# Kernel optimization log

Measured on AMD Instinct MI355X. Metric: run time of the kernel, lower is better.

Reference implementation:

```python
import jax, jax.numpy as jnp
import numpy as np

B, D, H, O = 8192, 1024, 1024, 1024
LN_EPS = 1e-6  # flax LayerNorm default


def setup_inputs() -> dict:
    key = jax.random.key(0)
    ks = jax.random.split(key, 18)
    s_i = 1.0 / np.sqrt(D)  # lecun_normal-ish scale, fan_in = D
    s_h = 1.0 / np.sqrt(H)
    inp = {
        "x": jax.random.normal(ks[0], (B, D), jnp.float32),
        "h": jax.random.normal(ks[1], (B, H), jnp.float32),
        # input projections (use_bias=True)
        "Wir": jax.random.normal(ks[2], (D, H), jnp.float32) * s_i,
        "bir": jax.random.normal(ks[3], (H,), jnp.float32) * 0.01,
        "Wiz": jax.random.normal(ks[4], (D, H), jnp.float32) * s_i,
        "biz": jnp.zeros((H,), jnp.float32),  # chrono_init with T_min=None -> zeros
        "Win": jax.random.normal(ks[5], (D, H), jnp.float32) * s_i,
        "bin_": jax.random.normal(ks[6], (H,), jnp.float32) * 0.01,
        # hidden projections (hr, hz: no bias; hn: bias)
        "Whr": jax.random.normal(ks[7], (H, H), jnp.float32) * s_h,
        "Whz": jax.random.normal(ks[8], (H, H), jnp.float32) * s_h,
        "Whn": jax.random.normal(ks[9], (H, H), jnp.float32) * s_h,
        "bhn": jax.random.normal(ks[10], (H,), jnp.float32) * 0.01,
        # LayerNorm params
        "ln_scale": jnp.ones((H,), jnp.float32),
        "ln_bias": jnp.zeros((H,), jnp.float32),
        # readout
        "Wout": jax.random.normal(ks[11], (H, O), jnp.float32) * s_h,
        "bout": jax.random.normal(ks[12], (O,), jnp.float32) * 0.01,
    }
    return inp


def _layer_norm(x, scale, bias):
    mu = jnp.mean(x, axis=-1, keepdims=True)
    var = jnp.mean(jnp.square(x - mu), axis=-1, keepdims=True)
    return (x - mu) * jax.lax.rsqrt(var + LN_EPS) * scale + bias


def reference(x, h, Wir, bir, Wiz, biz, Win, bin_, Whr, Whz, Whn, bhn,
              ln_scale, ln_bias, Wout, bout):
    # GRU recurrence (stop_gradients='none' branch)
    r = jax.nn.sigmoid(x @ Wir + bir + h @ Whr)          # [B,H]
    z = jax.nn.sigmoid(x @ Wiz + biz + h @ Whz)          # [B,H]
    n = jnp.tanh(x @ Win + bin_ + r * (h @ Whn + bhn))   # [B,H]
    new_h = (1.0 - z) * n + z * h                        # [B,H]
    # readout: LayerNorm then Dense
    out = _layer_norm(new_h, ln_scale, ln_bias) @ Wout + bout  # [B,O]
    return new_h, out
```

## Files before the change

kernel.cpp:

```cpp
#include <hip/hip_runtime.h>
#include <math.h>

#define B_ 8192
#define H_ 1024
#define K2 2048

typedef __attribute__((ext_vector_type(8))) short bf16x8;
typedef __attribute__((ext_vector_type(4))) float f32x4;
typedef unsigned short u16;

__device__ __forceinline__ u16 f2bf(float f) {
  unsigned u = __float_as_uint(f);
  u += 0x7fffu + ((u >> 16) & 1u);
  return (u16)(u >> 16);
}
__device__ __forceinline__ float bf2f(u16 s) { return __uint_as_float(((unsigned)s) << 16); }

__global__ __launch_bounds__(256) void split_hl(const float* __restrict__ src,
                                                u16* __restrict__ hi, u16* __restrict__ lo,
                                                int col04) {
  const int n4 = B_ * H_ / 4;
  int i = blockIdx.x * blockDim.x + threadIdx.x;
  int stride = gridDim.x * blockDim.x;
  for (; i < n4; i += stride) {
    float4 v = reinterpret_cast<const float4*>(src)[i];
    int row = i >> 8;
    int c4 = i & 255;
    float c[4] = {v.x, v.y, v.z, v.w};
    u16 hh[4], ll[4];
#pragma unroll
    for (int j = 0; j < 4; j++) {
      hh[j] = f2bf(c[j]);
      ll[j] = f2bf(c[j] - bf2f(hh[j]));
    }
    ushort4 h4 = {hh[0], hh[1], hh[2], hh[3]};
    ushort4 l4 = {ll[0], ll[1], ll[2], ll[3]};
    size_t o4 = (size_t)row * (K2 / 4) + col04 + c4;
    reinterpret_cast<ushort4*>(hi)[o4] = h4;
    reinterpret_cast<ushort4*>(lo)[o4] = l4;
  }
}

__global__ __launch_bounds__(256) void transpose_hi(const float* __restrict__ W,
                                                    u16* __restrict__ Thi,
                                                    int K, int N, int ldo, int koff) {
  __shared__ float tile[32][33];
  int bx = blockIdx.x * 32;
  int by = blockIdx.y * 32;
  int tx = threadIdx.x, ty = threadIdx.y;
#pragma unroll
  for (int i = 0; i < 4; i++)
    tile[ty + i * 8][tx] = W[(size_t)(by + ty + i * 8) * N + bx + tx];
  __syncthreads();
#pragma unroll
  for (int i = 0; i < 4; i++) {
    float v = tile[tx][ty + i * 8];
    size_t o = (size_t)(bx + ty + i * 8) * ldo + koff + by + tx;
    Thi[o] = f2bf(v);
  }
}

#define BM 128
#define BN 128
#define BK 64

__device__ __forceinline__ void gload16(const void* g, void* l) {
  __builtin_amdgcn_global_load_lds((const __attribute__((address_space(1))) unsigned int*)g,
                                   (__attribute__((address_space(3))) unsigned int*)l,
                                   16, 0, 0);
}

__global__ __launch_bounds__(256, 3) void gemm3(const u16* __restrict__ Ahi,
                                                const u16* __restrict__ Alo, int lda,
                                                const u16* __restrict__ Bhi,
                                                const float* __restrict__ bias, float* C,
                                                int N, int K, int mode,
                                                const float* zbuf, const float* xnbuf,
                                                const float* hnbuf, const float* hbuf) {
  __shared__ u16 lds[3 * BM * BK];
  u16* sAh = lds;
  u16* sAl = lds + BM * BK;
  u16* sBh = lds + 2 * BM * BK;

  const int tid = threadIdx.x;
  const int lane = tid & 63;
  const int wv = tid >> 6;
  const int wr = wv >> 1, wc = wv & 1;
  const int fr = lane & 15;
  const int fs = lane >> 4;

  const int lin = blockIdx.y * gridDim.x + blockIdx.x;
  const int cpx = (gridDim.x * gridDim.y) >> 3;
  const int nlin = (lin & 7) * cpx + (lin >> 3);
  const int m0 = (nlin / gridDim.x) * BM;
  const int n0 = (nlin % gridDim.x) * BN;

  f32x4 acc[4][4] = {};

  for (int k0 = 0; k0 < K; k0 += BK) {
#pragma unroll
    for (int q = 0; q < 4; q++) {
      int idx = q * 256 + tid;
      int row = idx >> 3;
      int ls = (idx & 7) ^ (row & 7);
      size_t ga = (size_t)(m0 + row) * lda + k0 + ls * 8;
      size_t gb = (size_t)(n0 + row) * K + k0 + ls * 8;
      gload16(Ahi + ga, sAh + (size_t)idx * 8);
      gload16(Alo + ga, sAl + (size_t)idx * 8);
      gload16(Bhi + gb, sBh + (size_t)idx * 8);
    }
    __syncthreads();

#pragma unroll
    for (int kh = 0; kh < 2; kh++) {
      bf16x8 ah[4], al[4], bh[4];
#pragma unroll
      for (int i = 0; i < 4; i++) {
        int ar = wr * 64 + i * 16 + fr;
        int ao = ar * 64 + (((kh * 4 + fs) ^ (ar & 7)) << 3);
        ah[i] = *reinterpret_cast<const bf16x8*>(sAh + ao);
        al[i] = *reinterpret_cast<const bf16x8*>(sAl + ao);
        int br = wc * 64 + i * 16 + fr;
        int bo = br * 64 + (((kh * 4 + fs) ^ (br & 7)) << 3);
        bh[i] = *reinterpret_cast<const bf16x8*>(sBh + bo);
      }
#pragma unroll
      for (int mi = 0; mi < 4; mi++)
#pragma unroll
        for (int ni = 0; ni < 4; ni++) {
          acc[mi][ni] = __builtin_amdgcn_mfma_f32_16x16x32_bf16(ah[mi], bh[ni], acc[mi][ni], 0, 0, 0);
          acc[mi][ni] = __builtin_amdgcn_mfma_f32_16x16x32_bf16(al[mi], bh[ni], acc[mi][ni], 0, 0, 0);
        }
    }
    __syncthreads();
  }

#pragma unroll
  for (int mi = 0; mi < 4; mi++) {
    int grow = m0 + wr * 64 + mi * 16 + fs * 4;
#pragma unroll
    for (int ni = 0; ni < 4; ni++) {
      int gcol = n0 + wc * 64 + ni * 16 + fr;
      float bv = bias[gcol];
      if (mode == 0) {
#pragma unroll
        for (int j = 0; j < 4; j++)
          C[(size_t)(grow + j) * N + gcol] = acc[mi][ni][j] + bv;
      } else {
#pragma unroll
        for (int j = 0; j < 4; j++) {
          size_t idx = (size_t)(grow + j) * N + gcol;
          float z = 1.f / (1.f + expf(-zbuf[idx]));
          float r = 1.f / (1.f + expf(-(acc[mi][ni][j] + bv)));
          float n = tanhf(xnbuf[idx] + r * hnbuf[idx]);
          C[idx] = (1.f - z) * n + z * hbuf[idx];
        }
      }
    }
  }
}

__global__ __launch_bounds__(256) void ln_split(const float* __restrict__ src,
                                                const float* __restrict__ scale,
                                                const float* __restrict__ bias,
                                                u16* __restrict__ lhi, u16* __restrict__ llo) {
  int row = blockIdx.x, t = threadIdx.x;
  float4 vv = reinterpret_cast<const float4*>(src + (size_t)row * H_)[t];
  float v[4] = {vv.x, vv.y, vv.z, vv.w};
  float s = 0.f, s2 = 0.f;
#pragma unroll
  for (int i = 0; i < 4; i++) {
    s += v[i];
    s2 += v[i] * v[i];
  }
#pragma unroll
  for (int m = 32; m >= 1; m >>= 1) {
    s += __shfl_xor(s, m);
    s2 += __shfl_xor(s2, m);
  }
  __shared__ float red[8];
  int lane = t & 63, wv = t >> 6;
  if (lane == 0) {
    red[wv] = s;
    red[4 + wv] = s2;
  }
  __syncthreads();
  s = red[0] + red[1] + red[2] + red[3];
  s2 = red[4] + red[5] + red[6] + red[7];
  float mu = s * (1.f / H_);
  float var = s2 * (1.f / H_) - mu * mu;
  float inv = rsqrtf(var + 1e-6f);
  float4 sc = reinterpret_cast<const float4*>(scale)[t];
  float4 bi = reinterpret_cast<const float4*>(bias)[t];
  float scv[4] = {sc.x, sc.y, sc.z, sc.w};
  float biv[4] = {bi.x, bi.y, bi.z, bi.w};
  u16 hh[4], ll[4];
#pragma unroll
  for (int i = 0; i < 4; i++) {
    float y = (v[i] - mu) * inv * scv[i] + biv[i];
    hh[i] = f2bf(y);
    ll[i] = f2bf(y - bf2f(hh[i]));
  }
  ushort4 h4 = {hh[0], hh[1], hh[2], hh[3]};
  ushort4 l4 = {ll[0], ll[1], ll[2], ll[3]};
  reinterpret_cast<ushort4*>(lhi)[(size_t)row * 256 + t] = h4;
  reinterpret_cast<ushort4*>(llo)[(size_t)row * 256 + t] = l4;
}

extern "C" void kernel_launch(void* const* d_in, const int* in_sizes, int n_in,
                              void* d_out, int out_size, void* d_ws, size_t ws_size,
                              hipStream_t stream) {
  const float* x = (const float*)d_in[0];
  const float* h = (const float*)d_in[1];
  const float* Wir = (const float*)d_in[2];
  const float* bir = (const float*)d_in[3];
  const float* Wiz = (const float*)d_in[4];
  const float* biz = (const float*)d_in[5];
  const float* Win = (const float*)d_in[6];
  const float* bin_ = (const float*)d_in[7];
  const float* Whr = (const float*)d_in[8];
  const float* Whz = (const float*)d_in[9];
  const float* Whn = (const float*)d_in[10];
  const float* bhn = (const float*)d_in[11];
  const float* ln_scale = (const float*)d_in[12];
  const float* ln_bias = (const float*)d_in[13];
  const float* Wout = (const float*)d_in[14];
  const float* bout = (const float*)d_in[15];

  float* out_h = (float*)d_out;
  float* out_o = (float*)d_out + (size_t)B_ * H_;

  char* ws = (char*)d_ws;
  size_t off = 0;
  auto alloc = [&](size_t bytes) {
    void* p = ws + off;
    off += (bytes + 255) & ~(size_t)255;
    return p;
  };
  u16* xh_hi = (u16*)alloc((size_t)B_ * K2 * 2);
  u16* xh_lo = (u16*)alloc((size_t)B_ * K2 * 2);
  u16* WrT_hi = (u16*)alloc((size_t)H_ * K2 * 2);
  u16* WzT_hi = (u16*)alloc((size_t)H_ * K2 * 2);
  u16* WinT_hi = (u16*)alloc((size_t)H_ * H_ * 2);
  u16* WhnT_hi = (u16*)alloc((size_t)H_ * H_ * 2);
  u16* WoT_hi = (u16*)alloc((size_t)H_ * H_ * 2);
  float* HN = (float*)alloc((size_t)B_ * H_ * 4);
  u16* ln_hi = xh_hi;
  u16* ln_lo = xh_lo;

  split_hl<<<2048, 256, 0, stream>>>(x, xh_hi, xh_lo, 0);
  split_hl<<<2048, 256, 0, stream>>>(h, xh_hi, xh_lo, 256);

  dim3 tb(32, 8), tg(H_ / 32, H_ / 32);
  transpose_hi<<<tg, tb, 0, stream>>>(Wir, WrT_hi, H_, H_, K2, 0);
  transpose_hi<<<tg, tb, 0, stream>>>(Whr, WrT_hi, H_, H_, K2, 1024);
  transpose_hi<<<tg, tb, 0, stream>>>(Wiz, WzT_hi, H_, H_, K2, 0);
  transpose_hi<<<tg, tb, 0, stream>>>(Whz, WzT_hi, H_, H_, K2, 1024);
  transpose_hi<<<tg, tb, 0, stream>>>(Win, WinT_hi, H_, H_, H_, 0);
  transpose_hi<<<tg, tb, 0, stream>>>(Whn, WhnT_hi, H_, H_, H_, 0);
  transpose_hi<<<tg, tb, 0, stream>>>(Wout, WoT_hi, H_, H_, H_, 0);

  dim3 gg(H_ / BN, B_ / BM);
  gemm3<<<gg, 256, 0, stream>>>(xh_hi, xh_lo, K2, WzT_hi, biz, out_h, H_, K2, 0,
                                nullptr, nullptr, nullptr, nullptr);
  gemm3<<<gg, 256, 0, stream>>>(xh_hi, xh_lo, K2, WinT_hi, bin_, out_o, H_, H_, 0,
                                nullptr, nullptr, nullptr, nullptr);
  gemm3<<<gg, 256, 0, stream>>>(xh_hi + H_, xh_lo + H_, K2, WhnT_hi, bhn, HN, H_, H_, 0,
                                nullptr, nullptr, nullptr, nullptr);
  gemm3<<<gg, 256, 0, stream>>>(xh_hi, xh_lo, K2, WrT_hi, bir, out_h, H_, K2, 1,
                                out_h, out_o, HN, h);
  ln_split<<<B_, 256, 0, stream>>>(out_h, ln_scale, ln_bias, ln_hi, ln_lo);
  gemm3<<<gg, 256, 0, stream>>>(ln_hi, ln_lo, H_, WoT_hi, bout, out_o, H_, H_, 0,
                                nullptr, nullptr, nullptr, nullptr);
}
```

Baseline: 433.9 us.

## Fuse r and z gate GEMMs into one kernel sharing A tiles

Replaces the separate z-gate GEMM and r-gate GEMM with a single kernel that computes both accumulators from the same loaded A (hi/lo) tiles, then applies the full GRU epilogue. This removes one pass over the 8192x2048 activation operand and the write and reread of the intermediate z buffer. In exchange it doubles the accumulator registers and LDS per block, lowering the occupancy bound from 3 to 2 blocks per CU and risking register pressure or spills.

```diff
diff --git a/kernel.cpp b/kernel.cpp
--- a/kernel.cpp
+++ b/kernel.cpp
@@ -74,9 +74,7 @@
                                                 const u16* __restrict__ Alo, int lda,
                                                 const u16* __restrict__ Bhi,
                                                 const float* __restrict__ bias, float* C,
-                                                int N, int K, int mode,
-                                                const float* zbuf, const float* xnbuf,
-                                                const float* hnbuf, const float* hbuf) {
+                                                int N, int K) {
   __shared__ u16 lds[3 * BM * BK];
   u16* sAh = lds;
   u16* sAl = lds + BM * BK;
@@ -142,19 +140,102 @@
     for (int ni = 0; ni < 4; ni++) {
       int gcol = n0 + wc * 64 + ni * 16 + fr;
       float bv = bias[gcol];
-      if (mode == 0) {
-#pragma unroll
-        for (int j = 0; j < 4; j++)
-          C[(size_t)(grow + j) * N + gcol] = acc[mi][ni][j] + bv;
-      } else {
-#pragma unroll
-        for (int j = 0; j < 4; j++) {
-          size_t idx = (size_t)(grow + j) * N + gcol;
-          float z = 1.f / (1.f + expf(-zbuf[idx]));
-          float r = 1.f / (1.f + expf(-(acc[mi][ni][j] + bv)));
-          float n = tanhf(xnbuf[idx] + r * hnbuf[idx]);
-          C[idx] = (1.f - z) * n + z * hbuf[idx];
+#pragma unroll
+      for (int j = 0; j < 4; j++)
+        C[(size_t)(grow + j) * N + gcol] = acc[mi][ni][j] + bv;
+    }
+  }
+}
+
+__global__ __launch_bounds__(256, 2) void gemm_rz(const u16* __restrict__ Ahi,
+                                                  const u16* __restrict__ Alo,
+                                                  const u16* __restrict__ Br,
+                                                  const u16* __restrict__ Bz,
+                                                  const float* __restrict__ bir,
+                                                  const float* __restrict__ biz,
+                                                  const float* __restrict__ xn,
+                                                  const float* __restrict__ hn,
+                                                  const float* __restrict__ h,
+                                                  float* __restrict__ outh) {
+  __shared__ u16 lds[4 * BM * BK];
+  u16* sAh = lds;
+  u16* sAl = lds + BM * BK;
+  u16* sBr = lds + 2 * BM * BK;
+  u16* sBz = lds + 3 * BM * BK;
+
+  const int tid = threadIdx.x;
+  const int lane = tid & 63;
+  const int wv = tid >> 6;
+  const int wr = wv >> 1, wc = wv & 1;
+  const int fr = lane & 15;
+  const int fs = lane >> 4;
+
+  const int lin = blockIdx.y * gridDim.x + blockIdx.x;
+  const int cpx = (gridDim.x * gridDim.y) >> 3;
+  const int nlin = (lin & 7) * cpx + (lin >> 3);
+  const int m0 = (nlin / gridDim.x) * BM;
+  const int n0 = (nlin % gridDim.x) * BN;
+
+  f32x4 accR[4][4] = {};
+  f32x4 accZ[4][4] = {};
+
+  for (int k0 = 0; k0 < K2; k0 += BK) {
+#pragma unroll
+    for (int q = 0; q < 4; q++) {
+      int idx = q * 256 + tid;
+      int row = idx >> 3;
+      int ls = (idx & 7) ^ (row & 7);
+      size_t ga = (size_t)(m0 + row) * K2 + k0 + ls * 8;
+      size_t gb = (size_t)(n0 + row) * K2 + k0 + ls * 8;
+      gload16(Ahi + ga, sAh + (size_t)idx * 8);
+      gload16(Alo + ga, sAl + (size_t)idx * 8);
+      gload16(Br + gb, sBr + (size_t)idx * 8);
+      gload16(Bz + gb, sBz + (size_t)idx * 8);
+    }
+    __syncthreads();
+
+#pragma unroll
+    for (int kh = 0; kh < 2; kh++) {
+      bf16x8 ah[4], al[4], br[4], bz[4];
+#pragma unroll
+      for (int i = 0; i < 4; i++) {
+        int ar = wr * 64 + i * 16 + fr;
+        int ao = ar * 64 + (((kh * 4 + fs) ^ (ar & 7)) << 3);
+        ah[i] = *reinterpret_cast<const bf16x8*>(sAh + ao);
+        al[i] = *reinterpret_cast<const bf16x8*>(sAl + ao);
+        int brr = wc * 64 + i * 16 + fr;
+        int bo = brr * 64 + (((kh * 4 + fs) ^ (brr & 7)) << 3);
+        br[i] = *reinterpret_cast<const bf16x8*>(sBr + bo);
+        bz[i] = *reinterpret_cast<const bf16x8*>(sBz + bo);
+      }
+#pragma unroll
+      for (int mi = 0; mi < 4; mi++)
+#pragma unroll
+        for (int ni = 0; ni < 4; ni++) {
+          accR[mi][ni] = __builtin_amdgcn_mfma_f32_16x16x32_bf16(ah[mi], br[ni], accR[mi][ni], 0, 0, 0);
+          accR[mi][ni] = __builtin_amdgcn_mfma_f32_16x16x32_bf16(al[mi], br[ni], accR[mi][ni], 0, 0, 0);
+          accZ[mi][ni] = __builtin_amdgcn_mfma_f32_16x16x32_bf16(ah[mi], bz[ni], accZ[mi][ni], 0, 0, 0);
+          accZ[mi][ni] = __builtin_amdgcn_mfma_f32_16x16x32_bf16(al[mi], bz[ni], accZ[mi][ni], 0, 0, 0);
         }
+    }
+    __syncthreads();
+  }
+
+#pragma unroll
+  for (int mi = 0; mi < 4; mi++) {
+    int grow = m0 + wr * 64 + mi * 16 + fs * 4;
+#pragma unroll
+    for (int ni = 0; ni < 4; ni++) {
+      int gcol = n0 + wc * 64 + ni * 16 + fr;
+      float brv = bir[gcol];
+      float bzv = biz[gcol];
+#pragma unroll
+      for (int j = 0; j < 4; j++) {
+        size_t idx = (size_t)(grow + j) * H_ + gcol;
+        float r = 1.f / (1.f + expf(-(accR[mi][ni][j] + brv)));
+        float z = 1.f / (1.f + expf(-(accZ[mi][ni][j] + bzv)));
+        float n = tanhf(xn[idx] + r * hn[idx]);
+        outh[idx] = (1.f - z) * n + z * h[idx];
       }
     }
   }
@@ -261,15 +342,10 @@
   transpose_hi<<<tg, tb, 0, stream>>>(Wout, WoT_hi, H_, H_, H_, 0);
 
   dim3 gg(H_ / BN, B_ / BM);
-  gemm3<<<gg, 256, 0, stream>>>(xh_hi, xh_lo, K2, WzT_hi, biz, out_h, H_, K2, 0,
-                                nullptr, nullptr, nullptr, nullptr);
-  gemm3<<<gg, 256, 0, stream>>>(xh_hi, xh_lo, K2, WinT_hi, bin_, out_o, H_, H_, 0,
-                                nullptr, nullptr, nullptr, nullptr);
-  gemm3<<<gg, 256, 0, stream>>>(xh_hi + H_, xh_lo + H_, K2, WhnT_hi, bhn, HN, H_, H_, 0,
-                                nullptr, nullptr, nullptr, nullptr);
-  gemm3<<<gg, 256, 0, stream>>>(xh_hi, xh_lo, K2, WrT_hi, bir, out_h, H_, K2, 1,
-                                out_h, out_o, HN, h);
+  gemm3<<<gg, 256, 0, stream>>>(xh_hi, xh_lo, K2, WinT_hi, bin_, out_o, H_, H_);
+  gemm3<<<gg, 256, 0, stream>>>(xh_hi + H_, xh_lo + H_, K2, WhnT_hi, bhn, HN, H_, H_);
+  gemm_rz<<<gg, 256, 0, stream>>>(xh_hi, xh_lo, WrT_hi, WzT_hi, bir, biz,
+                                  out_o, HN, h, out_h);
   ln_split<<<B_, 256, 0, stream>>>(out_h, ln_scale, ln_bias, ln_hi, ln_lo);
-  gemm3<<<gg, 256, 0, stream>>>(ln_hi, ln_lo, H_, WoT_hi, bout, out_o, H_, H_, 0,
-                                nullptr, nullptr, nullptr, nullptr);
-}
+  gemm3<<<gg, 256, 0, stream>>>(ln_hi, ln_lo, H_, WoT_hi, bout, out_o, H_, H_);
+}
```

After: 436.4 us. Within noise of the previous version (+0.6%).
